# Performance work log

Hardware: AMD Instinct MI355X
Metric: run time of the kernel (lower is better)

Reference implementation:

```python
import jax, jax.numpy as jnp
import numpy as np

IN_SIZE, HID_SIZE, OUT_SIZE = 256, 512, 256
BATCH, NSTEPS = 64, 2048


def setup_inputs() -> dict:
    key = jax.random.key(0)
    ks = jax.random.split(key, 6)
    s_ih = 1.0 / np.sqrt(IN_SIZE)
    s_hh = 1.0 / np.sqrt(HID_SIZE)
    return {
        "input": jax.random.normal(ks[0], (BATCH, NSTEPS, IN_SIZE), dtype=jnp.float32),
        "w_ih": jax.random.uniform(ks[1], (HID_SIZE, IN_SIZE), jnp.float32, -s_ih, s_ih),
        "w_hh": jax.random.uniform(ks[2], (HID_SIZE, HID_SIZE), jnp.float32, -s_hh, s_hh),
        "b_h": jax.random.uniform(ks[3], (HID_SIZE,), jnp.float32, -s_hh, s_hh),
        "w_out": jax.random.uniform(ks[4], (OUT_SIZE, HID_SIZE), jnp.float32, -s_hh, s_hh),
        "b_out": jax.random.uniform(ks[5], (OUT_SIZE,), jnp.float32, -s_hh, s_hh),
    }


def reference(input, w_ih, w_hh, b_h, w_out, b_out):
    # Vanilla RNN recurrence (delay=1 in the original forward) + linear readout.
    # h_t = tanh(x_t W_ih^T + h_{t-1} W_hh^T + b_h);  y_t = h_t W_out^T + b_out
    batch = input.shape[0]
    h0 = jnp.zeros((batch, w_hh.shape[0]), dtype=input.dtype)
    # Precompute input projections for all steps in one big GEMM (same math).
    x_proj = jnp.einsum("bti,hi->bth", input, w_ih) + b_h  # [B, T, H]

    def step(h, xp_t):
        h_new = jnp.tanh(xp_t + h @ w_hh.T)
        return h_new, h_new

    _, hs = jax.lax.scan(step, h0, jnp.swapaxes(x_proj, 0, 1))  # hs: [T, B, H]
    hs = jnp.swapaxes(hs, 0, 1)  # [B, T, H]
    outputs = jnp.einsum("bth,oh->bto", hs, w_out) + b_out  # [B, T, O]
    return outputs
```

## Files before the change

kernel.cpp:

```cpp
#include <hip/hip_runtime.h>


typedef _Float16 f16;
typedef __attribute__((ext_vector_type(2))) _Float16 half2_t;
typedef __attribute__((ext_vector_type(4))) float float4_t;

#define NIN    256
#define NHID   512
#define NOUT   256
#define NBATCH 64
#define NT     2048

#define FL4(p) (*reinterpret_cast<const float4_t*>(p))
#define LOADA(p)     __hip_atomic_load((p), __ATOMIC_RELAXED, __HIP_MEMORY_SCOPE_AGENT)
#define STOREA(p, v) __hip_atomic_store((p), (v), __ATOMIC_RELAXED, __HIP_MEMORY_SCOPE_AGENT)

#define LDS_BAR() do {                                              \
    asm volatile("s_waitcnt lgkmcnt(0)\n\ts_barrier" ::: "memory"); \
    __builtin_amdgcn_sched_barrier(0);                              \
  } while (0)

#if __has_builtin(__builtin_amdgcn_fdot2)
__device__ __forceinline__ float fdot2f(half2_t a, half2_t b, float c) {
  return __builtin_amdgcn_fdot2(a, b, c, false);
}
#else
__device__ __forceinline__ float fdot2f(half2_t a, half2_t b, float c) {
  return c + (float)a.x * (float)b.x + (float)a.y * (float)b.y;
}
#endif

__device__ __forceinline__ float tanh_fast(float x) {
  float e = __expf(2.0f * x);
  return 1.0f - 2.0f / (e + 1.0f);
}

__device__ unsigned long long g_pub[NBATCH][2][NHID];

__global__ __launch_bounds__(256) void k_zero() {
  ((unsigned long long*)g_pub)[blockIdx.x * 256 + threadIdx.x] = 0ull;
}

__global__ __launch_bounds__(256) void k_inproj(
    const float* __restrict__ x, const float* __restrict__ w,
    const float* __restrict__ bias, float* __restrict__ xplo, float* __restrict__ xphi)
{
  __shared__ float xs[32][260];
  __shared__ float wsT[8][520];
  const int t = threadIdx.x;
  const int m0 = blockIdx.x * 32;
  const int mthr = t & 3;
  const int nthr = t >> 2;

  #pragma unroll
  for (int r = 0; r < 8; ++r) {
    int f = (t + 256 * r) * 4;
    int row = f >> 8, col = f & 255;
    *(float4_t*)&xs[row][col] =
        *reinterpret_cast<const float4_t*>(x + (size_t)(m0 + row) * NIN + col);
  }

  float acc[8][8];
  #pragma unroll
  for (int nn = 0; nn < 8; ++nn) {
    float bv = bias[nthr * 8 + nn];
    #pragma unroll
    for (int mm = 0; mm < 8; ++mm) acc[nn][mm] = bv;
  }

  for (int kc = 0; kc < 32; ++kc) {
    __syncthreads();
    #pragma unroll
    for (int r = 0; r < 4; ++r) {
      int f = (t + 256 * r) * 4;
      int n = f >> 3, k0 = f & 7;
      float4_t v = *reinterpret_cast<const float4_t*>(w + (size_t)n * NIN + kc * 8 + k0);
      #pragma unroll
      for (int j = 0; j < 4; ++j) wsT[k0 + j][n] = v[j];
    }
    __syncthreads();
    #pragma unroll
    for (int kp = 0; kp < 8; ++kp) {
      float4_t wv0 = *(const float4_t*)&wsT[kp][nthr * 8];
      float4_t wv1 = *(const float4_t*)&wsT[kp][nthr * 8 + 4];
      #pragma unroll
      for (int mm = 0; mm < 8; ++mm) {
        float xv = xs[mthr * 8 + mm][kc * 8 + kp];
        acc[0][mm] = fmaf(wv0.x, xv, acc[0][mm]);
        acc[1][mm] = fmaf(wv0.y, xv, acc[1][mm]);
        acc[2][mm] = fmaf(wv0.z, xv, acc[2][mm]);
        acc[3][mm] = fmaf(wv0.w, xv, acc[3][mm]);
        acc[4][mm] = fmaf(wv1.x, xv, acc[4][mm]);
        acc[5][mm] = fmaf(wv1.y, xv, acc[5][mm]);
        acc[6][mm] = fmaf(wv1.z, xv, acc[6][mm]);
        acc[7][mm] = fmaf(wv1.w, xv, acc[7][mm]);
      }
    }
  }

  const int n0 = nthr * 8;
  float* dst = (n0 < 256) ? (xplo + n0) : (xphi + (n0 - 256));
  #pragma unroll
  for (int mm = 0; mm < 8; ++mm) {
    int m = m0 + mthr * 8 + mm;
    float4_t o0 = {acc[0][mm], acc[1][mm], acc[2][mm], acc[3][mm]};
    float4_t o1 = {acc[4][mm], acc[5][mm], acc[6][mm], acc[7][mm]};
    *reinterpret_cast<float4_t*>(dst + (size_t)m * 256)     = o0;
    *reinterpret_cast<float4_t*>(dst + (size_t)m * 256 + 4) = o1;
  }
}

__global__ __launch_bounds__(512, 1) void k_recur(
    const float* __restrict__ whh, float* outbuf, float* wsbuf)
{
  __shared__ __align__(16) float hl[2][NHID];
  __shared__ __align__(16) float pacc[2][8][128];
  const int g = blockIdx.x;
  const int b = (g >> 5) * 8 + (g & 7);
  const int q = (g >> 3) & 3;
  const int t = threadIdx.x;
  const int js = t & 63;
  const int ks = t >> 6;
  const int r0 = q * 128 + js * 2, r1 = r0 + 1;
  const bool ownw = (ks >> 1) == q;

  float4_t w0[16], w1[16];
  #pragma unroll
  for (int i = 0; i < 16; ++i) {
    w0[i] = FL4(whh + (size_t)r0 * NHID + ks * 64 + i * 4);
    w1[i] = FL4(whh + (size_t)r1 * NHID + ks * 64 + i * 4);
  }

  float* xp = ((t < 256) ? (outbuf + t) : (wsbuf + (t - 256))) + (size_t)b * NT * 256;
  float xq0 = 0.f, xq1 = 0.f;
  if (ownw) { xq0 = xp[0]; xq1 = xp[256]; }

  hl[0][t] = 0.0f;
  __syncthreads();

  for (int s = 0; s < NT; ++s) {
    const int par = s & 1;

    if (!ownw && s > 0) {
      unsigned long long pv = LOADA(&g_pub[b][(s - 1) & 1][t]);
      while ((unsigned)(pv >> 32) < (unsigned)s)
        pv = LOADA(&g_pub[b][(s - 1) & 1][t]);
      hl[par][t] = __builtin_bit_cast(float, (unsigned)pv);
      asm volatile("s_waitcnt lgkmcnt(0)" ::: "memory");
      __builtin_amdgcn_sched_barrier(0);
    }

    float4_t a0 = {0.f,0.f,0.f,0.f}, a1 = {0.f,0.f,0.f,0.f};
    float4_t b0 = {0.f,0.f,0.f,0.f}, b1 = {0.f,0.f,0.f,0.f};
    {
      const float4_t* h4 = (const float4_t*)&hl[par][ks * 64];
      #pragma unroll
      for (int i = 0; i < 16; i += 2) {
        float4_t hA = h4[i], hB = h4[i + 1];
        a0 += w0[i] * hA;  a1 += w0[i + 1] * hB;
        b0 += w1[i] * hA;  b1 += w1[i + 1] * hB;
      }
    }
    float4_t av = a0 + a1, bv = b0 + b1;
    pacc[par][ks][js * 2]     = (av.x + av.y) + (av.z + av.w);
    pacc[par][ks][js * 2 + 1] = (bv.x + bv.y) + (bv.z + bv.w);
    LDS_BAR();

    if (ownw) {
      const int lr = t & 127;
      float sum = ((pacc[par][0][lr] + pacc[par][1][lr]) +
                   (pacc[par][2][lr] + pacc[par][3][lr])) +
                  ((pacc[par][4][lr] + pacc[par][5][lr]) +
                   (pacc[par][6][lr] + pacc[par][7][lr]));
      float h = tanh_fast(sum + xq0);
      STOREA(&g_pub[b][par][t],
             ((unsigned long long)(unsigned)(s + 1) << 32) |
             (unsigned long long)__builtin_bit_cast(unsigned, h));
      hl[par ^ 1][t] = h;
      xp[(size_t)s * 256] = h;
      xq0 = xq1;
      if (s + 2 < NT) xq1 = xp[(size_t)(s + 2) * 256];
    }
  }
}

__global__ __launch_bounds__(256) void k_outproj(
    const float* hlo, const float* hhi, const float* __restrict__ w,
    const float* __restrict__ bias, float* out)
{
  __shared__ half2_t xs[32][258];
  __shared__ half2_t ws[256][19];
  const int t = threadIdx.x;
  const int m0 = blockIdx.x * 32;
  const int nthr = t >> 2;
  const int mthr = t & 3;

  #pragma unroll
  for (int r = 0; r < 16; ++r) {
    int f = (t + 256 * r) * 4;
    int row = f >> 9, col = f & 511;
    const float* src = (col < 256) ? (hlo + (size_t)(m0 + row) * 256 + col)
                                   : (hhi + (size_t)(m0 + row) * 256 + (col - 256));
    float4_t v = *reinterpret_cast<const float4_t*>(src);
    xs[row][(col >> 1)]     = half2_t{(f16)v.x, (f16)v.y};
    xs[row][(col >> 1) + 1] = half2_t{(f16)v.z, (f16)v.w};
  }

  float acc[4][8];
  #pragma unroll
  for (int nn = 0; nn < 4; ++nn) {
    float bv = bias[nthr * 4 + nn];
    #pragma unroll
    for (int mm = 0; mm < 8; ++mm) acc[nn][mm] = bv;
  }

  for (int kc = 0; kc < 16; ++kc) {
    __syncthreads();
    #pragma unroll
    for (int r = 0; r < 8; ++r) {
      int f = (t + 256 * r) * 4;
      int row = f >> 5, col = f & 31;
      float4_t v = *reinterpret_cast<const float4_t*>(w + (size_t)row * NHID + kc * 32 + col);
      ws[row][(col >> 1)]     = half2_t{(f16)v.x, (f16)v.y};
      ws[row][(col >> 1) + 1] = half2_t{(f16)v.z, (f16)v.w};
    }
    __syncthreads();
    #pragma unroll
    for (int kp = 0; kp < 16; ++kp) {
      half2_t wv[4], xv[8];
      #pragma unroll
      for (int nn = 0; nn < 4; ++nn) wv[nn] = ws[nthr * 4 + nn][kp];
      #pragma unroll
      for (int mm = 0; mm < 8; ++mm) xv[mm] = xs[mthr * 8 + mm][kc * 16 + kp];
      #pragma unroll
      for (int nn = 0; nn < 4; ++nn)
        #pragma unroll
        for (int mm = 0; mm < 8; ++mm)
          acc[nn][mm] = fdot2f(wv[nn], xv[mm], acc[nn][mm]);
    }
  }

  #pragma unroll
  for (int mm = 0; mm < 8; ++mm) {
    int m = m0 + mthr * 8 + mm;
    float4_t o = {acc[0][mm], acc[1][mm], acc[2][mm], acc[3][mm]};
    *reinterpret_cast<float4_t*>(out + (size_t)m * NOUT + nthr * 4) = o;
  }
}

extern "C" void kernel_launch(void* const* d_in, const int* in_sizes, int n_in,
                              void* d_out, int out_size, void* d_ws, size_t ws_size,
                              hipStream_t stream) {
  (void)in_sizes; (void)n_in; (void)ws_size; (void)out_size;
  const float* x     = (const float*)d_in[0];
  const float* w_ih  = (const float*)d_in[1];
  const float* w_hh  = (const float*)d_in[2];
  const float* b_h   = (const float*)d_in[3];
  const float* w_out = (const float*)d_in[4];
  const float* b_out = (const float*)d_in[5];

  float* outb = (float*)d_out;
  float* wsb  = (float*)d_ws;

  k_zero   <<<256, 256, 0, stream>>>();
  k_inproj <<<(NBATCH * NT) / 32, 256, 0, stream>>>(x, w_ih, b_h, outb, wsb);
  k_recur  <<<256, 512, 0, stream>>>(w_hh, outb, wsb);
  k_outproj<<<(NBATCH * NT) / 32, 256, 0, stream>>>(outb, wsb, w_out, b_out, outb);
}
```

Before: 4.256 ms.

## Restructure RNN recurrence to quad-lane row split with DPP reduction and single barrier

Each block now gives every hidden row to four adjacent lanes, each covering a 128-wide K slice. The partial sums are reduced with DPP cross-lane adds, which replaces the LDS partial-sum array and one of the per-step barriers. Lanes poll for remote hidden-state chunks at the end of the step and write them into a padded LDS layout, with s_sleep added to the spin loop, so each step has one barrier. The cost is that only one lane in four does tanh and stores, and the sleep can add latency to the cross-block handoff.

Measured after the change: 5.531 ms. 1.3x slower.

```diff
diff --git a/kernel.cpp b/kernel.cpp
--- a/kernel.cpp
+++ b/kernel.cpp
@@ -113,74 +113,66 @@
 __global__ __launch_bounds__(512, 1) void k_recur(
     const float* __restrict__ whh, float* outbuf, float* wsbuf)
 {
-  __shared__ __align__(16) float hl[2][NHID];
-  __shared__ __align__(16) float pacc[2][8][128];
+  __shared__ __align__(16) float hl[2][4][132];
   const int g = blockIdx.x;
   const int b = (g >> 5) * 8 + (g & 7);
   const int q = (g >> 3) & 3;
   const int t = threadIdx.x;
-  const int js = t & 63;
-  const int ks = t >> 6;
-  const int r0 = q * 128 + js * 2, r1 = r0 + 1;
-  const bool ownw = (ks >> 1) == q;
-
-  float4_t w0[16], w1[16];
-  #pragma unroll
-  for (int i = 0; i < 16; ++i) {
-    w0[i] = FL4(whh + (size_t)r0 * NHID + ks * 64 + i * 4);
-    w1[i] = FL4(whh + (size_t)r1 * NHID + ks * 64 + i * 4);
-  }
-
-  float* xp = ((t < 256) ? (outbuf + t) : (wsbuf + (t - 256))) + (size_t)b * NT * 256;
+  const int kq = t & 3;
+  const int ri = t >> 2;
+  const int r  = q * 128 + ri;
+  const bool lead = (kq == 0);
+  const bool prb  = (kq != q);
+
+  float4_t w[32];
+  #pragma unroll
+  for (int i = 0; i < 32; ++i)
+    w[i] = FL4(whh + (size_t)r * NHID + kq * 128 + i * 4);
+
+  float* xp = nullptr;
   float xq0 = 0.f, xq1 = 0.f;
-  if (ownw) { xq0 = xp[0]; xq1 = xp[256]; }
-
-  hl[0][t] = 0.0f;
+  if (lead) {
+    xp = ((q < 2) ? (outbuf + r) : (wsbuf + (r - 256))) + (size_t)b * NT * 256;
+    xq0 = xp[0]; xq1 = xp[256];
+  }
+
+  hl[0][t >> 7][t & 127] = 0.0f;
   __syncthreads();
 
   for (int s = 0; s < NT; ++s) {
     const int par = s & 1;
 
-    if (!ownw && s > 0) {
-      unsigned long long pv = LOADA(&g_pub[b][(s - 1) & 1][t]);
-      while ((unsigned)(pv >> 32) < (unsigned)s)
-        pv = LOADA(&g_pub[b][(s - 1) & 1][t]);
-      hl[par][t] = __builtin_bit_cast(float, (unsigned)pv);
-      asm volatile("s_waitcnt lgkmcnt(0)" ::: "memory");
-      __builtin_amdgcn_sched_barrier(0);
-    }
-
-    float4_t a0 = {0.f,0.f,0.f,0.f}, a1 = {0.f,0.f,0.f,0.f};
-    float4_t b0 = {0.f,0.f,0.f,0.f}, b1 = {0.f,0.f,0.f,0.f};
-    {
-      const float4_t* h4 = (const float4_t*)&hl[par][ks * 64];
-      #pragma unroll
-      for (int i = 0; i < 16; i += 2) {
-        float4_t hA = h4[i], hB = h4[i + 1];
-        a0 += w0[i] * hA;  a1 += w0[i + 1] * hB;
-        b0 += w1[i] * hA;  b1 += w1[i + 1] * hB;
-      }
-    }
-    float4_t av = a0 + a1, bv = b0 + b1;
-    pacc[par][ks][js * 2]     = (av.x + av.y) + (av.z + av.w);
-    pacc[par][ks][js * 2 + 1] = (bv.x + bv.y) + (bv.z + bv.w);
-    LDS_BAR();
-
-    if (ownw) {
-      const int lr = t & 127;
-      float sum = ((pacc[par][0][lr] + pacc[par][1][lr]) +
-                   (pacc[par][2][lr] + pacc[par][3][lr])) +
-                  ((pacc[par][4][lr] + pacc[par][5][lr]) +
-                   (pacc[par][6][lr] + pacc[par][7][lr]));
+    const float4_t* h4 = (const float4_t*)&hl[par][kq][0];
+    float4_t a = {0.f,0.f,0.f,0.f}, c = {0.f,0.f,0.f,0.f};
+    #pragma unroll
+    for (int i = 0; i < 32; i += 2) { a += w[i] * h4[i]; c += w[i + 1] * h4[i + 1]; }
+    float4_t sv = a + c;
+    float sum = (sv.x + sv.y) + (sv.z + sv.w);
+    int xi;
+    xi = __builtin_amdgcn_update_dpp(0, __builtin_bit_cast(int, sum), 0xB1, 0xF, 0xF, true);
+    sum += __builtin_bit_cast(float, xi);
+    xi = __builtin_amdgcn_update_dpp(0, __builtin_bit_cast(int, sum), 0x4E, 0xF, 0xF, true);
+    sum += __builtin_bit_cast(float, xi);
+
+    if (lead) {
       float h = tanh_fast(sum + xq0);
-      STOREA(&g_pub[b][par][t],
+      STOREA(&g_pub[b][par][r],
              ((unsigned long long)(unsigned)(s + 1) << 32) |
              (unsigned long long)__builtin_bit_cast(unsigned, h));
-      hl[par ^ 1][t] = h;
+      hl[par ^ 1][q][ri] = h;
       xp[(size_t)s * 256] = h;
       xq0 = xq1;
       if (s + 2 < NT) xq1 = xp[(size_t)(s + 2) * 256];
     }
+    if (prb && s + 1 < NT) {
+      unsigned long long pv = LOADA(&g_pub[b][par][kq * 128 + ri]);
+      while ((unsigned)(pv >> 32) < (unsigned)(s + 1)) {
+        __builtin_amdgcn_s_sleep(1);
+        pv = LOADA(&g_pub[b][par][kq * 128 + ri]);
+      }
+      hl[par ^ 1][kq][ri] = __builtin_bit_cast(float, (unsigned)pv);
+    }
+    LDS_BAR();
   }
 }
 
```

## Interleave two batch rows per recurrence block to overlap cross-block waits

Applied to the files above, without the earlier changes.

Each recurrence block now handles two batch rows instead of one, halving the grid to 128 blocks. It staggers the matvec, spin-wait on peer-published hidden state, and finalize phases of the two rows so that one row's compute hides the other's inter-block latency. Polling loads for the next step are issued early, right after publishing. This adds LDS buffers and more complex barrier sequencing, and halves the number of active CUs.

After: 5.509 ms. +29.4%, slower.

```diff
diff --git a/kernel.cpp b/kernel.cpp
--- a/kernel.cpp
+++ b/kernel.cpp
@@ -113,16 +113,18 @@
 __global__ __launch_bounds__(512, 1) void k_recur(
     const float* __restrict__ whh, float* outbuf, float* wsbuf)
 {
-  __shared__ __align__(16) float hl[2][NHID];
-  __shared__ __align__(16) float pacc[2][8][128];
+  __shared__ __align__(16) float hlA[2][NHID], hlB[2][NHID];
+  __shared__ __align__(16) float paccA[8][128], paccB[8][128];
   const int g = blockIdx.x;
-  const int b = (g >> 5) * 8 + (g & 7);
   const int q = (g >> 3) & 3;
+  const int G = (g & 7) + 8 * (g >> 5);
+  const int bA = 2 * G, bB = 2 * G + 1;
   const int t = threadIdx.x;
   const int js = t & 63;
   const int ks = t >> 6;
   const int r0 = q * 128 + js * 2, r1 = r0 + 1;
-  const bool ownw = (ks >> 1) == q;
+  const bool ownk = (ks >> 1) == q;
+  const int prow = (q * 128 + 128 + t) & 511;
 
   float4_t w0[16], w1[16];
   #pragma unroll
@@ -131,57 +133,85 @@
     w1[i] = FL4(whh + (size_t)r1 * NHID + ks * 64 + i * 4);
   }
 
-  float* xp = ((t < 256) ? (outbuf + t) : (wsbuf + (t - 256))) + (size_t)b * NT * 256;
-  float xq0 = 0.f, xq1 = 0.f;
-  if (ownw) { xq0 = xp[0]; xq1 = xp[256]; }
-
-  hl[0][t] = 0.0f;
+  float* xpA = nullptr;
+  float* xpB = nullptr;
+  float xqA0 = 0.f, xqA1 = 0.f, xqB0 = 0.f, xqB1 = 0.f;
+  if (t < 128) {
+    float* base = (q < 2) ? (outbuf + q * 128) : (wsbuf + (q - 2) * 128);
+    xpA = base + (size_t)bA * NT * 256 + t;
+    xpB = base + (size_t)bB * NT * 256 + t;
+    xqA0 = xpA[0]; xqA1 = xpA[256];
+    xqB0 = xpB[0]; xqB1 = xpB[256];
+  }
+
+  hlA[0][t] = 0.0f; hlB[0][t] = 0.0f;
   __syncthreads();
+
+  unsigned long long pvA = 0, pvB = 0;
+
+  #define FMA_BODY(HL, PACC)                                                     \
+  {                                                                              \
+    const float4_t* h4 = (const float4_t*)&HL[par][ks * 64];                     \
+    float4_t a0 = {0.f,0.f,0.f,0.f}, a1 = {0.f,0.f,0.f,0.f};                     \
+    float4_t b0 = {0.f,0.f,0.f,0.f}, b1 = {0.f,0.f,0.f,0.f};                     \
+    _Pragma("unroll")                                                            \
+    for (int i = 0; i < 16; i += 2) {                                            \
+      float4_t hA = h4[i], hB = h4[i + 1];                                       \
+      a0 += w0[i] * hA;  a1 += w0[i + 1] * hB;                                   \
+      b0 += w1[i] * hA;  b1 += w1[i + 1] * hB;                                   \
+    }                                                                            \
+    float4_t av = a0 + a1, bv = b0 + b1;                                         \
+    PACC[ks][js * 2]     = (av.x + av.y) + (av.z + av.w);                        \
+    PACC[ks][js * 2 + 1] = (bv.x + bv.y) + (bv.z + bv.w);                        \
+  }
+
+  #define FIN_BODY(BB, HL, PACC, XP, XQ0, XQ1, PV)                               \
+  {                                                                              \
+    if (t < 128) {                                                               \
+      float sum = PACC[0][t];                                                    \
+      _Pragma("unroll")                                                          \
+      for (int k2 = 1; k2 < 8; ++k2) sum += PACC[k2][t];                         \
+      float h = tanh_fast(sum + XQ0);                                            \
+      STOREA(&g_pub[BB][par][q * 128 + t],                                       \
+             ((unsigned long long)(unsigned)(s + 1) << 32) |                     \
+             (unsigned long long)__builtin_bit_cast(unsigned, h));               \
+      HL[par ^ 1][q * 128 + t] = h;                                              \
+      XP[(size_t)s * 256] = h;                                                   \
+      XQ0 = XQ1;                                                                 \
+      if (s + 2 < NT) XQ1 = XP[(size_t)(s + 2) * 256];                           \
+    }                                                                            \
+    if (s + 1 < NT && t < 384)                                                   \
+      PV = LOADA(&g_pub[BB][(s + 1) & 1 ^ 1][prow]);      \
+  }
 
   for (int s = 0; s < NT; ++s) {
     const int par = s & 1;
 
-    if (!ownw && s > 0) {
-      unsigned long long pv = LOADA(&g_pub[b][(s - 1) & 1][t]);
-      while ((unsigned)(pv >> 32) < (unsigned)s)
-        pv = LOADA(&g_pub[b][(s - 1) & 1][t]);
-      hl[par][t] = __builtin_bit_cast(float, (unsigned)pv);
-      asm volatile("s_waitcnt lgkmcnt(0)" ::: "memory");
-      __builtin_amdgcn_sched_barrier(0);
-    }
-
-    float4_t a0 = {0.f,0.f,0.f,0.f}, a1 = {0.f,0.f,0.f,0.f};
-    float4_t b0 = {0.f,0.f,0.f,0.f}, b1 = {0.f,0.f,0.f,0.f};
-    {
-      const float4_t* h4 = (const float4_t*)&hl[par][ks * 64];
-      #pragma unroll
-      for (int i = 0; i < 16; i += 2) {
-        float4_t hA = h4[i], hB = h4[i + 1];
-        a0 += w0[i] * hA;  a1 += w0[i + 1] * hB;
-        b0 += w1[i] * hA;  b1 += w1[i + 1] * hB;
-      }
-    }
-    float4_t av = a0 + a1, bv = b0 + b1;
-    pacc[par][ks][js * 2]     = (av.x + av.y) + (av.z + av.w);
-    pacc[par][ks][js * 2 + 1] = (bv.x + bv.y) + (bv.z + bv.w);
+    if (ownk) FMA_BODY(hlA, paccA);
+    if (s > 0 && t < 384) {
+      while ((unsigned)(pvA >> 32) < (unsigned)s)
+        pvA = LOADA(&g_pub[bA][(s - 1) & 1][prow]);
+      hlA[par][prow] = __builtin_bit_cast(float, (unsigned)pvA);
+    }
     LDS_BAR();
 
-    if (ownw) {
-      const int lr = t & 127;
-      float sum = ((pacc[par][0][lr] + pacc[par][1][lr]) +
-                   (pacc[par][2][lr] + pacc[par][3][lr])) +
-                  ((pacc[par][4][lr] + pacc[par][5][lr]) +
-                   (pacc[par][6][lr] + pacc[par][7][lr]));
-      float h = tanh_fast(sum + xq0);
-      STOREA(&g_pub[b][par][t],
-             ((unsigned long long)(unsigned)(s + 1) << 32) |
-             (unsigned long long)__builtin_bit_cast(unsigned, h));
-      hl[par ^ 1][t] = h;
-      xp[(size_t)s * 256] = h;
-      xq0 = xq1;
-      if (s + 2 < NT) xq1 = xp[(size_t)(s + 2) * 256];
-    }
-  }
+    if (ownk) FMA_BODY(hlB, paccB);
+    if (!ownk) FMA_BODY(hlA, paccA);
+    if (s > 0 && t < 384) {
+      while ((unsigned)(pvB >> 32) < (unsigned)s)
+        pvB = LOADA(&g_pub[bB][(s - 1) & 1][prow]);
+      hlB[par][prow] = __builtin_bit_cast(float, (unsigned)pvB);
+    }
+    LDS_BAR();
+
+    FIN_BODY(bA, hlA, paccA, xpA, xqA0, xqA1, pvA)
+    if (!ownk) FMA_BODY(hlB, paccB);
+    LDS_BAR();
+
+    FIN_BODY(bB, hlB, paccB, xpB, xqB0, xqB1, pvB)
+  }
+  #undef FMA_BODY
+  #undef FIN_BODY
 }
 
 __global__ __launch_bounds__(256) void k_outproj(
@@ -264,6 +294,6 @@
 
   k_zero   <<<256, 256, 0, stream>>>();
   k_inproj <<<(NBATCH * NT) / 32, 256, 0, stream>>>(x, w_ih, b_h, outb, wsb);
-  k_recur  <<<256, 512, 0, stream>>>(w_hh, outb, wsb);
+  k_recur  <<<128, 512, 0, stream>>>(w_hh, outb, wsb);
   k_outproj<<<(NBATCH * NT) / 32, 256, 0, stream>>>(outb, wsb, w_out, b_out, outb);
 }
```
